# Kernel optimization log

Hardware: AMD Instinct MI355X
Metric: run time of the kernel (lower is better)

The kernel has to match this reference:

```python
import jax, jax.numpy as jnp
import numpy as np

D_MODEL = 1024
N_HEADS = 16
D_K = D_MODEL // N_HEADS
B, S = 2, 2048
NEG = -1.0e9


def setup_inputs() -> dict:
    key = jax.random.key(0)
    ks = jax.random.split(key, 12)
    sc = 1.0 / np.sqrt(D_MODEL)
    inp = {
        'query': jax.random.normal(ks[0], (B, S, D_MODEL), jnp.float32),
        'key': jax.random.normal(ks[1], (B, S, D_MODEL), jnp.float32),
        'value': jax.random.normal(ks[2], (B, S, D_MODEL), jnp.float32),
        # causal mask, broadcast over batch: 1 = attend, 0 = masked
        'mask': jnp.broadcast_to(jnp.tril(jnp.ones((S, S), jnp.int32)), (B, S, S)),
        'wq': jax.random.normal(ks[3], (D_MODEL, D_MODEL), jnp.float32) * sc,
        'bq': jnp.zeros((D_MODEL,), jnp.float32),
        'wk': jax.random.normal(ks[4], (D_MODEL, D_MODEL), jnp.float32) * sc,
        'bk': jnp.zeros((D_MODEL,), jnp.float32),
        'wv': jax.random.normal(ks[5], (D_MODEL, D_MODEL), jnp.float32) * sc,
        'bv': jnp.zeros((D_MODEL,), jnp.float32),
        'wo': jax.random.normal(ks[6], (D_MODEL, D_MODEL), jnp.float32) * sc,
        'bo': jnp.zeros((D_MODEL,), jnp.float32),
    }
    return inp


def reference(query, key, value, mask, wq, bq, wk, bk, wv, bv, wo, bo):
    b, sq, _ = query.shape
    sk = key.shape[1]
    # linear projections, split into heads: [B, H, S, d_k]
    def proj(x, w, bias, s):
        return (x @ w + bias).reshape(b, s, N_HEADS, D_K).transpose(0, 2, 1, 3)
    Q = proj(query, wq, bq, sq)
    K = proj(key, wk, bk, sk)
    V = proj(value, wv, bv, sk)
    # scaled dot-product attention with full score matrix [B, H, Sq, Sk]
    scores = jnp.einsum('bhqd,bhkd->bhqk', Q, K) / np.sqrt(D_K)
    scores = jnp.where(mask[:, None, :, :] == 0, NEG, scores)
    attn = jax.nn.softmax(scores, axis=-1)
    ctx = jnp.einsum('bhqk,bhkd->bhqd', attn, V)
    ctx = ctx.transpose(0, 2, 1, 3).reshape(b, sq, D_MODEL)
    return ctx @ wo + bo
```

## Files before the change

kernel.cpp:

```cpp
#include <hip/hip_runtime.h>
#include <stdint.h>

#define AS1 __attribute__((address_space(1)))
#define AS3 __attribute__((address_space(3)))

typedef __attribute__((ext_vector_type(8))) __bf16 bf16x8;
typedef __attribute__((ext_vector_type(4))) float f32x4;
typedef __attribute__((ext_vector_type(4))) unsigned int u32x4;
typedef __attribute__((ext_vector_type(2))) unsigned int u32x2;

static __device__ __forceinline__ void gload16(const void* g, void* l) {
    __builtin_amdgcn_global_load_lds((AS1 void*)(uintptr_t)g, (AS3 void*)l, 16, 0, 0);
}

static __device__ __forceinline__ unsigned cvt_pk_bf16(float lo, float hi) {
    unsigned r;
    asm volatile("v_cvt_pk_bf16_f32 %0, %1, %2" : "=v"(r) : "v"(lo), "v"(hi));
    return r;
}
static __device__ __forceinline__ unsigned short f2bf(float f) {
    return (unsigned short)(cvt_pk_bf16(f, 0.f) & 0xffffu);
}

static __device__ __forceinline__ f32x4 mfma16(bf16x8 a, bf16x8 b, f32x4 c) {
    return __builtin_amdgcn_mfma_f32_16x16x32_bf16(a, b, c, 0, 0, 0);
}

__global__ __launch_bounds__(256) void k_wtrans4(const float* __restrict__ w0,
                                                 const float* __restrict__ w1,
                                                 const float* __restrict__ w2,
                                                 const float* __restrict__ w3,
                                                 unsigned short* __restrict__ o0,
                                                 unsigned short* __restrict__ o1,
                                                 unsigned short* __restrict__ o2,
                                                 unsigned short* __restrict__ o3) {
    const float* W;
    unsigned short* Wt;
    switch (blockIdx.z) {
        case 0: W = w0; Wt = o0; break;
        case 1: W = w1; Wt = o1; break;
        case 2: W = w2; Wt = o2; break;
        default: W = w3; Wt = o3; break;
    }
    __shared__ unsigned short tile[64][72];
    const int tid = threadIdx.x;
    const int k0 = blockIdx.x * 64, n0 = blockIdx.y * 64;
#pragma unroll
    for (int j = 0; j < 4; ++j) {
        int c = j * 256 + tid;
        int kr = c >> 4, c4 = c & 15;
        f32x4 v = *(const f32x4*)(W + (size_t)(k0 + kr) * 1024 + n0 + c4 * 4);
#pragma unroll
        for (int e = 0; e < 4; ++e) tile[c4 * 4 + e][kr] = f2bf(v[e]);
    }
    __syncthreads();
#pragma unroll
    for (int j = 0; j < 2; ++j) {
        int c = j * 256 + tid;
        int nr = c >> 3, kc = c & 7;
        union { unsigned short s[8]; u32x4 v; } t;
#pragma unroll
        for (int e = 0; e < 8; ++e) t.s[e] = tile[nr][kc * 8 + e];
        *(u32x4*)(Wt + (size_t)(n0 + nr) * 1024 + k0 + kc * 8) = t.v;
    }
}

template <int A_F32, int OUT_F32>
static __device__ __forceinline__ void gemm_body(const void* __restrict__ Ap,
                                                 const unsigned short* __restrict__ Bt,
                                                 const float* __restrict__ bias,
                                                 void* __restrict__ Cp,
                                                 int M, int N, int K, float cscale,
                                                 char* smem) {
    constexpr int ASZ = A_F32 ? 16384 : 8192;
    char* sA = smem;
    char* sB = smem + 2 * ASZ;
    const int tid = threadIdx.x;
    const int wave = tid >> 6, lane = tid & 63, g = lane >> 4, l16 = lane & 15;
    const int wm = wave & 1, wn = wave >> 1;
    const int m0 = blockIdx.x * 64, n0 = blockIdx.y * 128;

    f32x4 acc[2][4];
#pragma unroll
    for (int i = 0; i < 2; ++i)
#pragma unroll
        for (int j = 0; j < 4; ++j) acc[i][j] = (f32x4){0.f, 0.f, 0.f, 0.f};

    auto STAGE = [&](int k0, int buf) {
        if constexpr (A_F32) {
            const float* A = (const float*)Ap;
            char* dst = sA + buf * ASZ;
#pragma unroll
            for (int j = 0; j < 4; ++j) {
                int c = j * 256 + tid;
                int row = c >> 4, w = c & 15, kc = w ^ (row & 15);
                gload16(A + (size_t)(m0 + row) * K + k0 + kc * 4, dst + c * 16);
            }
        } else {
            const unsigned short* A = (const unsigned short*)Ap;
            char* dst = sA + buf * ASZ;
#pragma unroll
            for (int j = 0; j < 2; ++j) {
                int c = j * 256 + tid;
                int row = c >> 3, w = c & 7, kc = w ^ (row & 7);
                gload16(A + (size_t)(m0 + row) * K + k0 + kc * 8, dst + c * 16);
            }
        }
        char* dst = sB + buf * 16384;
#pragma unroll
        for (int j = 0; j < 4; ++j) {
            int c = j * 256 + tid;
            int row = c >> 3, w = c & 7, kc = w ^ (row & 7);
            gload16(Bt + (size_t)(n0 + row) * K + k0 + kc * 8, dst + c * 16);
        }
    };

    const int nkt = K >> 6;
    STAGE(0, 0);
    __syncthreads();
    int cur = 0;
#pragma unroll 1
    for (int kt = 0; kt < nkt; ++kt) {
        if (kt + 1 < nkt) STAGE((kt + 1) << 6, cur ^ 1);
        const char* sAc = sA + cur * ASZ;
        const char* sBc = sB + cur * 16384;
#pragma unroll
        for (int ks = 0; ks < 2; ++ks) {
            bf16x8 af[2];
#pragma unroll
            for (int mi = 0; mi < 2; ++mi) {
                int row = wm * 32 + mi * 16 + l16;
                if constexpr (A_F32) {
                    int c0 = (ks * 8 + g * 2) ^ (row & 15);
                    int c1 = (ks * 8 + g * 2 + 1) ^ (row & 15);
                    f32x4 lo = *(const f32x4*)(sAc + row * 256 + c0 * 16);
                    f32x4 hi = *(const f32x4*)(sAc + row * 256 + c1 * 16);
                    union { unsigned u[4]; bf16x8 v; } cv;
                    cv.u[0] = cvt_pk_bf16(lo[0], lo[1]);
                    cv.u[1] = cvt_pk_bf16(lo[2], lo[3]);
                    cv.u[2] = cvt_pk_bf16(hi[0], hi[1]);
                    cv.u[3] = cvt_pk_bf16(hi[2], hi[3]);
                    af[mi] = cv.v;
                } else {
                    int c = (ks * 4 + g) ^ (row & 7);
                    af[mi] = *(const bf16x8*)(sAc + row * 128 + c * 16);
                }
            }
#pragma unroll
            for (int ni = 0; ni < 4; ++ni) {
                int row = wn * 64 + ni * 16 + l16;
                int c = (ks * 4 + g) ^ (row & 7);
                bf16x8 bfr = *(const bf16x8*)(sBc + row * 128 + c * 16);
#pragma unroll
                for (int mi = 0; mi < 2; ++mi)
                    acc[mi][ni] = mfma16(af[mi], bfr, acc[mi][ni]);
            }
        }
        __syncthreads();
        cur ^= 1;
    }
#pragma unroll
    for (int ni = 0; ni < 4; ++ni) {
        int col = n0 + wn * 64 + ni * 16 + l16;
        float bn = bias[col];
#pragma unroll
        for (int mi = 0; mi < 2; ++mi) {
            int rbase = m0 + wm * 32 + mi * 16 + g * 4;
#pragma unroll
            for (int r = 0; r < 4; ++r) {
                float v = (acc[mi][ni][r] + bn) * cscale;
                if constexpr (OUT_F32)
                    ((float*)Cp)[(size_t)(rbase + r) * N + col] = v;
                else
                    ((unsigned short*)Cp)[(size_t)(rbase + r) * N + col] = f2bf(v);
            }
        }
    }
}

__global__ __launch_bounds__(256) void k_gemm_qkv(
    const float* __restrict__ q, const float* __restrict__ k, const float* __restrict__ v,
    const unsigned short* __restrict__ Wq, const unsigned short* __restrict__ Wk,
    const unsigned short* __restrict__ Wv,
    const float* __restrict__ bq, const float* __restrict__ bk, const float* __restrict__ bv,
    unsigned short* __restrict__ Q2, unsigned short* __restrict__ K2,
    unsigned short* __restrict__ V2) {
    extern __shared__ __align__(16) char smem[];
    const float* A; const unsigned short* Bt; const float* bias; unsigned short* C; float sc;
    switch (blockIdx.z) {
        case 0:  A = q; Bt = Wq; bias = bq; C = Q2; sc = 0.18033688011112042f; break;
        case 1:  A = k; Bt = Wk; bias = bk; C = K2; sc = 1.0f; break;
        default: A = v; Bt = Wv; bias = bv; C = V2; sc = 1.0f; break;
    }
    gemm_body<1, 0>(A, Bt, bias, C, 4096, 1024, 1024, sc, smem);
}

__global__ __launch_bounds__(256) void k_gemm_o(const unsigned short* __restrict__ ctx,
                                                const unsigned short* __restrict__ Wo,
                                                const float* __restrict__ bo,
                                                float* __restrict__ out) {
    extern __shared__ __align__(16) char smem[];
    gemm_body<0, 1>(ctx, Wo, bo, out, 4096, 1024, 1024, 1.0f, smem);
}

__global__ __launch_bounds__(256) void k_vtrans(const unsigned short* __restrict__ V2,
                                                unsigned short* __restrict__ Vt) {
    __shared__ unsigned short tile[64][72];
    const int tid = threadIdx.x;
    const int s0 = blockIdx.x * 64;
    const int bh = blockIdx.y, b = bh >> 4, h = bh & 15;
#pragma unroll
    for (int j = 0; j < 2; ++j) {
        int c = j * 256 + tid;
        int sr = c >> 3, dc = c & 7;
        union { u32x4 v; unsigned short s[8]; } t;
        t.v = *(const u32x4*)(V2 + (size_t)(b * 2048 + s0 + sr) * 1024 + h * 64 + dc * 8);
#pragma unroll
        for (int e = 0; e < 8; ++e) tile[dc * 8 + e][sr] = t.s[e];
    }
    __syncthreads();
#pragma unroll
    for (int j = 0; j < 2; ++j) {
        int c = j * 256 + tid;
        int dr = c >> 3, sc = c & 7;
        union { unsigned short s[8]; u32x4 v; } t;
#pragma unroll
        for (int e = 0; e < 8; ++e) t.s[e] = tile[dr][sc * 8 + e];
        *(u32x4*)(Vt + ((size_t)bh * 64 + dr) * 2048 + s0 + sc * 8) = t.v;
    }
}

__global__ __launch_bounds__(128) void k_attn(const unsigned short* __restrict__ Q2,
                                              const unsigned short* __restrict__ K2,
                                              const unsigned short* __restrict__ Vt,
                                              unsigned short* __restrict__ ctx) {
    __shared__ __align__(16) char sK[8192];
    __shared__ __align__(16) char sV[2][8192];
    __shared__ __align__(16) char sP[2][2048];

    const int tid = threadIdx.x, w = tid >> 6, lane = tid & 63;
    const int g = lane >> 4, l16 = lane & 15;
    const int bid = blockIdx.x;
    const int xcd = bid & 7, j = bid >> 3;
    const int bh = xcd * 4 + (j & 3);
    const int t = 63 - (j >> 2);
    const int b = bh >> 4, h = bh & 15;
    const int swzl = (l16 & 7) << 4;

    const int r0 = tid >> 3;
    const int sc0 = (tid & 7) ^ (r0 & 7);
    const unsigned short* ksrc = K2 + (size_t)(b * 2048 + r0) * 1024 + h * 64 + sc0 * 8;
    const unsigned short* vsrc = Vt + ((size_t)bh * 64 + r0) * 2048 + sc0 * 8;
    char* const myp = sP[w];

    const int wq0 = t * 32 + w * 16;
    const int qg = wq0 + l16;

    const unsigned short* qp = Q2 + (size_t)(b * 2048 + wq0 + l16) * 1024 + h * 64;
    bf16x8 qf0 = *(const bf16x8*)(qp + g * 8);
    bf16x8 qf1 = *(const bf16x8*)(qp + 32 + g * 8);

    f32x4 accO[4];
#pragma unroll
    for (int i = 0; i < 4; ++i) accO[i] = (f32x4){0.f, 0.f, 0.f, 0.f};
    float m = 0.f, lsum = 0.f;

    const int nkv = (t >> 1) + 1;
    const int diag = t >> 1;
#pragma unroll
    for (int rr = 0; rr < 4; ++rr) {
        gload16(ksrc + (size_t)(rr * 16) * 1024, sK + rr * 2048 + tid * 16);
        gload16(vsrc + (size_t)(rr * 16) * 2048, sV[0] + rr * 2048 + tid * 16);
    }
    __syncthreads();

#pragma unroll 1
    for (int kt = 0; kt < nkv; ++kt) {
        const int cur = kt & 1;
        const int kv0 = kt * 64;
        float s[16];
        __builtin_amdgcn_s_setprio(1);
#pragma unroll
        for (int blk = 0; blk < 4; ++blk) {
            const int rl = blk * 16 + l16;
            const char* krow = sK + rl * 128;
            bf16x8 kf0 = *(const bf16x8*)(krow + ((g << 4) ^ swzl));
            bf16x8 kf1 = *(const bf16x8*)(krow + (((4 + g) << 4) ^ swzl));
            f32x4 a = (f32x4){0.f, 0.f, 0.f, 0.f};
            a = mfma16(kf0, qf0, a);
            a = mfma16(kf1, qf1, a);
#pragma unroll
            for (int rr = 0; rr < 4; ++rr) s[blk * 4 + rr] = a[rr];
        }
        __builtin_amdgcn_s_setprio(0);
        __syncthreads();
        if (kt + 1 < nkv) {
#pragma unroll
            for (int rr = 0; rr < 4; ++rr) {
                gload16(ksrc + (size_t)(kv0 + 64 + rr * 16) * 1024, sK + rr * 2048 + tid * 16);
                gload16(vsrc + (size_t)(rr * 16) * 2048 + (kv0 + 64), sV[cur ^ 1] + rr * 2048 + tid * 16);
            }
        }
        if (kt == diag) {
#pragma unroll
            for (int j2 = 0; j2 < 16; ++j2) {
                int kvg = kv0 + (j2 >> 2) * 16 + g * 4 + (j2 & 3);
                if (kvg > qg) s[j2] = -1e9f;
            }
        }
        float ps = 0.f;
        unsigned pk[8];
#pragma unroll
        for (int j2 = 0; j2 < 8; ++j2) {
            float p0 = __builtin_exp2f(s[2 * j2] - m);
            float p1 = __builtin_exp2f(s[2 * j2 + 1] - m);
            ps += p0 + p1;
            pk[j2] = cvt_pk_bf16(p0, p1);
        }
        if (__any(ps > 16777216.f)) {
            float c1 = fmaxf(fmaxf(s[0], s[1]), s[2]);
            c1 = fmaxf(fmaxf(c1, s[3]), s[4]);
            c1 = fmaxf(fmaxf(c1, s[5]), s[6]);
            c1 = fmaxf(c1, s[7]);
            float c2 = fmaxf(fmaxf(s[8], s[9]), s[10]);
            c2 = fmaxf(fmaxf(c2, s[11]), s[12]);
            c2 = fmaxf(fmaxf(c2, s[13]), s[14]);
            c2 = fmaxf(c2, s[15]);
            float mx = fmaxf(c1, c2);
            mx = fmaxf(mx, __shfl_xor(mx, 16));
            mx = fmaxf(mx, __shfl_xor(mx, 32));
            float mnew = fmaxf(m, mx);
            float scl = __builtin_exp2f(m - mnew);
            lsum *= scl;
#pragma unroll
            for (int dt = 0; dt < 4; ++dt) accO[dt] = accO[dt] * scl;
            m = mnew;
            ps = 0.f;
#pragma unroll
            for (int j2 = 0; j2 < 8; ++j2) {
                float p0 = __builtin_exp2f(s[2 * j2] - m);
                float p1 = __builtin_exp2f(s[2 * j2 + 1] - m);
                ps += p0 + p1;
                pk[j2] = cvt_pk_bf16(p0, p1);
            }
        }
        lsum += ps;
#pragma unroll
        for (int blk = 0; blk < 4; ++blk) {
            u32x2 pw = {pk[blk * 2], pk[blk * 2 + 1]};
            *(u32x2*)(myp + l16 * 128 + ((blk * 32 + g * 8) ^ swzl)) = pw;
        }
        __builtin_amdgcn_s_setprio(1);
#pragma unroll
        for (int kvh = 0; kvh < 2; ++kvh) {
            bf16x8 pf = *(const bf16x8*)(myp + l16 * 128 + ((kvh * 64 + g * 16) ^ swzl));
#pragma unroll
            for (int dt = 0; dt < 4; ++dt) {
                const int rv = dt * 16 + l16;
                bf16x8 vf = *(const bf16x8*)(sV[cur] + rv * 128 + (((kvh * 4 + g) << 4) ^ swzl));
                accO[dt] = mfma16(vf, pf, accO[dt]);
            }
        }
        __builtin_amdgcn_s_setprio(0);
        __syncthreads();
    }
    float v = lsum;
    v += __shfl_xor(v, 16);
    v += __shfl_xor(v, 32);
    float inv = 1.f / v;
    unsigned short* cp = ctx + (size_t)(b * 2048 + wq0 + l16) * 1024 + h * 64 + g * 4;
#pragma unroll
    for (int dt = 0; dt < 4; ++dt) {
        u32x2 o;
        o[0] = cvt_pk_bf16(accO[dt][0] * inv, accO[dt][1] * inv);
        o[1] = cvt_pk_bf16(accO[dt][2] * inv, accO[dt][3] * inv);
        *(u32x2*)(cp + dt * 16) = o;
    }
}

extern "C" void kernel_launch(void* const* d_in, const int* in_sizes, int n_in,
                              void* d_out, int out_size, void* d_ws, size_t ws_size,
                              hipStream_t stream) {
    const float* query = (const float*)d_in[0];
    const float* key   = (const float*)d_in[1];
    const float* value = (const float*)d_in[2];
    const float* wq = (const float*)d_in[4];
    const float* bq = (const float*)d_in[5];
    const float* wk = (const float*)d_in[6];
    const float* bk = (const float*)d_in[7];
    const float* wv = (const float*)d_in[8];
    const float* bv = (const float*)d_in[9];
    const float* wo = (const float*)d_in[10];
    const float* bo = (const float*)d_in[11];
    float* out = (float*)d_out;

    char* ws = (char*)d_ws;
    unsigned short* Wtq = (unsigned short*)ws;
    unsigned short* Wtk = Wtq + 1024 * 1024;
    unsigned short* Wtv = Wtk + 1024 * 1024;
    unsigned short* Wto = Wtv + 1024 * 1024;
    unsigned short* Q2  = Wto + 1024 * 1024;
    unsigned short* K2  = Q2 + 4096 * 1024;
    unsigned short* V2  = K2 + 4096 * 1024;
    unsigned short* Vt  = V2 + 4096 * 1024;
    unsigned short* ctx = Vt + 4096 * 1024;

    dim3 blk(256);
    k_wtrans4<<<dim3(16, 16, 4), blk, 0, stream>>>(wq, wk, wv, wo, Wtq, Wtk, Wtv, Wto);

    k_gemm_qkv<<<dim3(64, 8, 3), blk, 65536, stream>>>(query, key, value,
                                                       Wtq, Wtk, Wtv, bq, bk, bv,
                                                       Q2, K2, V2);

    k_vtrans<<<dim3(32, 32), blk, 0, stream>>>(V2, Vt);
    k_attn<<<dim3(2048), dim3(128), 0, stream>>>(Q2, K2, Vt, ctx);

    k_gemm_o<<<dim3(64, 8), blk, 49152, stream>>>(ctx, Wto, bo, out);
}
```

Baseline: 118.4 us.

## Rewrite QKV GEMM with 128x128 tiles and register-staged bf16 conversion of A

```diff
diff --git a/kernel.cpp b/kernel.cpp
--- a/kernel.cpp
+++ b/kernel.cpp
@@ -62,6 +62,107 @@
 #pragma unroll
         for (int e = 0; e < 8; ++e) t.s[e] = tile[nr][kc * 8 + e];
         *(u32x4*)(Wt + (size_t)(n0 + nr) * 1024 + k0 + kc * 8) = t.v;
+    }
+}
+
+__global__ __launch_bounds__(256, 3) void k_gemm_qkv(
+    const float* __restrict__ q, const float* __restrict__ k, const float* __restrict__ v,
+    const unsigned short* __restrict__ Wq, const unsigned short* __restrict__ Wk,
+    const unsigned short* __restrict__ Wv,
+    const float* __restrict__ bq, const float* __restrict__ bk, const float* __restrict__ bv,
+    unsigned short* __restrict__ Q2, unsigned short* __restrict__ K2,
+    unsigned short* __restrict__ V2) {
+    __shared__ __align__(16) char smem[32768];
+    char* sA = smem;
+    char* sB = smem + 16384;
+
+    const float* A; const unsigned short* Bt; const float* bias; unsigned short* C; float sc;
+    switch (blockIdx.z) {
+        case 0:  A = q; Bt = Wq; bias = bq; C = Q2; sc = 0.18033688011112042f; break;
+        case 1:  A = k; Bt = Wk; bias = bk; C = K2; sc = 1.0f; break;
+        default: A = v; Bt = Wv; bias = bv; C = V2; sc = 1.0f; break;
+    }
+    const int tid = threadIdx.x;
+    const int wave = tid >> 6, lane = tid & 63, g = lane >> 4, l16 = lane & 15;
+    const int wm = wave & 1, wn = wave >> 1;
+    const int m0 = blockIdx.x * 128, n0 = blockIdx.y * 128;
+    const int K = 1024, N = 1024;
+
+    const int arow = tid >> 1, ahalf = tid & 1;
+    const float* asrc = A + (size_t)(m0 + arow) * K + ahalf * 32;
+
+    f32x4 acc[4][4];
+#pragma unroll
+    for (int i = 0; i < 4; ++i)
+#pragma unroll
+        for (int j = 0; j < 4; ++j) acc[i][j] = (f32x4){0.f, 0.f, 0.f, 0.f};
+
+    f32x4 ar[8];
+#pragma unroll
+    for (int i = 0; i < 8; ++i) ar[i] = *(const f32x4*)(asrc + i * 4);
+
+    const int nkt = K >> 6;
+#pragma unroll 1
+    for (int kt = 0; kt < nkt; ++kt) {
+        const int k0 = kt << 6;
+        __syncthreads();
+#pragma unroll
+        for (int j = 0; j < 4; ++j) {
+            int c = j * 256 + tid;
+            int row = c >> 3, wch = c & 7, kc = wch ^ (row & 7);
+            gload16(Bt + (size_t)(n0 + row) * K + k0 + kc * 8, sB + c * 16);
+        }
+        unsigned aw[16];
+#pragma unroll
+        for (int i = 0; i < 8; ++i) {
+            aw[2 * i]     = cvt_pk_bf16(ar[i][0], ar[i][1]);
+            aw[2 * i + 1] = cvt_pk_bf16(ar[i][2], ar[i][3]);
+        }
+#pragma unroll
+        for (int j = 0; j < 4; ++j) {
+            u32x4 wv = {aw[4 * j], aw[4 * j + 1], aw[4 * j + 2], aw[4 * j + 3]};
+            int cw = ahalf * 4 + j;
+            *(u32x4*)(sA + arow * 128 + ((cw ^ (arow & 7)) << 4)) = wv;
+        }
+        if (kt + 1 < nkt) {
+#pragma unroll
+            for (int i = 0; i < 8; ++i)
+                ar[i] = *(const f32x4*)(asrc + ((kt + 1) << 6) + i * 4);
+        }
+        __syncthreads();
+#pragma unroll
+        for (int ks = 0; ks < 2; ++ks) {
+            bf16x8 af[4], bfr[4];
+#pragma unroll
+            for (int mi = 0; mi < 4; ++mi) {
+                int row = wm * 64 + mi * 16 + l16;
+                int c = (ks * 4 + g) ^ (row & 7);
+                af[mi] = *(const bf16x8*)(sA + row * 128 + c * 16);
+            }
+#pragma unroll
+            for (int ni = 0; ni < 4; ++ni) {
+                int row = wn * 64 + ni * 16 + l16;
+                int c = (ks * 4 + g) ^ (row & 7);
+                bfr[ni] = *(const bf16x8*)(sB + row * 128 + c * 16);
+            }
+#pragma unroll
+            for (int mi = 0; mi < 4; ++mi)
+#pragma unroll
+                for (int ni = 0; ni < 4; ++ni)
+                    acc[mi][ni] = mfma16(af[mi], bfr[ni], acc[mi][ni]);
+        }
+    }
+#pragma unroll
+    for (int ni = 0; ni < 4; ++ni) {
+        int col = n0 + wn * 64 + ni * 16 + l16;
+        float bn = bias[col];
+#pragma unroll
+        for (int mi = 0; mi < 4; ++mi) {
+            int rbase = m0 + wm * 64 + mi * 16 + g * 4;
+#pragma unroll
+            for (int r = 0; r < 4; ++r)
+                C[(size_t)(rbase + r) * N + col] = f2bf((acc[mi][ni][r] + bn) * sc);
+        }
     }
 }
 
@@ -178,23 +279,6 @@
     }
 }
 
-__global__ __launch_bounds__(256) void k_gemm_qkv(
-    const float* __restrict__ q, const float* __restrict__ k, const float* __restrict__ v,
-    const unsigned short* __restrict__ Wq, const unsigned short* __restrict__ Wk,
-    const unsigned short* __restrict__ Wv,
-    const float* __restrict__ bq, const float* __restrict__ bk, const float* __restrict__ bv,
-    unsigned short* __restrict__ Q2, unsigned short* __restrict__ K2,
-    unsigned short* __restrict__ V2) {
-    extern __shared__ __align__(16) char smem[];
-    const float* A; const unsigned short* Bt; const float* bias; unsigned short* C; float sc;
-    switch (blockIdx.z) {
-        case 0:  A = q; Bt = Wq; bias = bq; C = Q2; sc = 0.18033688011112042f; break;
-        case 1:  A = k; Bt = Wk; bias = bk; C = K2; sc = 1.0f; break;
-        default: A = v; Bt = Wv; bias = bv; C = V2; sc = 1.0f; break;
-    }
-    gemm_body<1, 0>(A, Bt, bias, C, 4096, 1024, 1024, sc, smem);
-}
-
 __global__ __launch_bounds__(256) void k_gemm_o(const unsigned short* __restrict__ ctx,
                                                 const unsigned short* __restrict__ Wo,
                                                 const float* __restrict__ bo,
@@ -408,9 +492,9 @@
     dim3 blk(256);
     k_wtrans4<<<dim3(16, 16, 4), blk, 0, stream>>>(wq, wk, wv, wo, Wtq, Wtk, Wtv, Wto);
 
-    k_gemm_qkv<<<dim3(64, 8, 3), blk, 65536, stream>>>(query, key, value,
-                                                       Wtq, Wtk, Wtv, bq, bk, bv,
-                                                       Q2, K2, V2);
+    k_gemm_qkv<<<dim3(32, 8, 3), blk, 0, stream>>>(query, key, value,
+                                                   Wtq, Wtk, Wtv, bq, bk, bv,
+                                                   Q2, K2, V2);
 
     k_vtrans<<<dim3(32, 32), blk, 0, stream>>>(V2, Vt);
     k_attn<<<dim3(2048), dim3(128), 0, stream>>>(Q2, K2, Vt, ctx);
```

New measurement: 134.0 us. 13.2% more time.
